# Performance work log

Hardware: AMD Instinct MI355X
Metric: run time of the kernel (lower is better)

Reference implementation:

```python
import jax, jax.numpy as jnp
import numpy as np

IN_FEATURES = 1024
OUT_FEATURES = 4096
POOL_K = 4
SCALE = 2.0
M = 32768


def setup_inputs() -> dict:
    key = jax.random.key(0)
    kx, kw, kb = jax.random.split(key, 3)
    bound = 1.0 / np.sqrt(IN_FEATURES)
    x = jax.random.normal(kx, (M, IN_FEATURES), dtype=jnp.float32)
    weight = jax.random.uniform(kw, (OUT_FEATURES, IN_FEATURES), dtype=jnp.float32, minval=-bound, maxval=bound)
    bias = jax.random.uniform(kb, (OUT_FEATURES,), dtype=jnp.float32, minval=-bound, maxval=bound)
    return {"x": x, "weight": weight, "bias": bias}


def _tanh_gelu(x):
    # tanh approximation of GELU, matching the Triton epilogue
    c = 0.7978845608028654  # sqrt(2/pi)
    return 0.5 * x * (1.0 + jnp.tanh(c * (x + 0.044715 * x * x * x)))


def reference(x, weight, bias):
    k = POOL_K
    n_pool = (OUT_FEATURES - k) // k + 1  # avgpool1d output length
    n_eff = n_pool * k
    # Fold AvgPool1d into weight/bias: avg over pooling groups
    w_pooled = weight[:n_eff].reshape(n_pool, k, IN_FEATURES).mean(axis=1)  # [N_pool, K]
    b_pooled = bias[:n_eff].reshape(n_pool, k).mean(axis=1)                  # [N_pool]
    y = jnp.einsum('mk,nk->mn', x, w_pooled) + b_pooled[None, :]             # [M, N_pool]
    y = _tanh_gelu(y) * SCALE
    return jnp.max(y, axis=1)  # [M]
```

## Files before the change

kernel.cpp:

```cpp
#include <hip/hip_runtime.h>
#include <hip/hip_bf16.h>

#define M_DIM 32768
#define K_DIM 1024
#define N_POOL 1024

#define BM 128
#define BN 128
#define BK 64

typedef __attribute__((ext_vector_type(8))) short bf16x8;
typedef __attribute__((ext_vector_type(4))) float f32x4;

typedef __attribute__((address_space(3))) unsigned int lds_uint;
typedef const __attribute__((address_space(1))) unsigned int g_uint;

__device__ __forceinline__ unsigned short f2bf(float f) {
    unsigned int u = __builtin_bit_cast(unsigned int, f);
    unsigned int lsb = (u >> 16) & 1u;
    u += 0x7fffu + lsb;
    return (unsigned short)(u >> 16);
}

__device__ __forceinline__ unsigned int f2bf2(float lo, float hi) {
    __hip_bfloat162 h2 = __float22bfloat162_rn(make_float2(lo, hi));
    union { __hip_bfloat162 h; unsigned int u; } c;
    c.h = h2;
    return c.u;
}

__global__ __launch_bounds__(256) void prep_kernel(
        const float* __restrict__ W, const float* __restrict__ b,
        unsigned short* __restrict__ wp, float* __restrict__ bp) {
    int n = blockIdx.x;
    int t = threadIdx.x;
    const float4* r0 = (const float4*)(W + (size_t)(4 * n + 0) * K_DIM);
    const float4* r1 = (const float4*)(W + (size_t)(4 * n + 1) * K_DIM);
    const float4* r2 = (const float4*)(W + (size_t)(4 * n + 2) * K_DIM);
    const float4* r3 = (const float4*)(W + (size_t)(4 * n + 3) * K_DIM);
    float4 a0 = r0[t], a1 = r1[t], a2 = r2[t], a3 = r3[t];
    float sx = (a0.x + a1.x + a2.x + a3.x) * 0.25f;
    float sy = (a0.y + a1.y + a2.y + a3.y) * 0.25f;
    float sz = (a0.z + a1.z + a2.z + a3.z) * 0.25f;
    float sw = (a0.w + a1.w + a2.w + a3.w) * 0.25f;
    ushort4 h;
    h.x = f2bf(sx); h.y = f2bf(sy); h.z = f2bf(sz); h.w = f2bf(sw);
    *(ushort4*)&wp[(size_t)n * K_DIM + t * 4] = h;
    if (t == 0)
        bp[n] = 0.25f * (b[4 * n] + b[4 * n + 1] + b[4 * n + 2] + b[4 * n + 3]);
}

__global__ __launch_bounds__(256, 2) void gemm_kernel(
        const float* __restrict__ x, const unsigned short* __restrict__ wp,
        const float* __restrict__ bp, float* __restrict__ partial) {
    __shared__ unsigned short As[BM * BK];
    __shared__ unsigned short Bs[BN * BK];

    int bid = blockIdx.x;
    int wg = (bid & 7) * 256 + (bid >> 3);
    int nblk = wg & 7;
    int mblk = wg >> 3;
    int m0 = mblk * BM;
    int n0 = nblk * BN;

    int tid = threadIdx.x;
    int lane = tid & 63;
    int wid = tid >> 6;
    int wr = wid >> 1, wc = wid & 1;

    f32x4 acc[4][4];
#pragma unroll
    for (int i = 0; i < 4; ++i)
#pragma unroll
        for (int j = 0; j < 4; ++j)
            acc[i][j] = (f32x4)(0.0f);

    const float4* xg = (const float4*)x;

    for (int kt = 0; kt < K_DIM / BK; ++kt) {
        __syncthreads();
#pragma unroll
        for (int i = 0; i < 4; ++i) {
            int ii = wid * 4 + i;
            int rsub = lane >> 3;
            int g = (lane & 7) ^ rsub;
            int n = n0 + ii * 8 + rsub;
            int kc = kt * BK + g * 8;
            __builtin_amdgcn_global_load_lds(
                (g_uint*)(wp + (size_t)n * K_DIM + kc),
                (lds_uint*)&Bs[ii * 512], 16, 0, 0);
        }
        float4 av[8];
#pragma unroll
        for (int j = 0; j < 4; ++j) {
            int f16 = j * 256 + tid;
            int r = f16 >> 3, c16 = f16 & 7;
            size_t base = (size_t)(m0 + r) * 256 + kt * 16 + c16 * 2;
            av[2 * j]     = xg[base];
            av[2 * j + 1] = xg[base + 1];
        }
#pragma unroll
        for (int j = 0; j < 4; ++j) {
            int f16 = j * 256 + tid;
            int r = f16 >> 3, c16 = f16 & 7;
            union { bf16x8 v; unsigned int u[4]; } pk;
            pk.u[0] = f2bf2(av[2 * j].x,     av[2 * j].y);
            pk.u[1] = f2bf2(av[2 * j].z,     av[2 * j].w);
            pk.u[2] = f2bf2(av[2 * j + 1].x, av[2 * j + 1].y);
            pk.u[3] = f2bf2(av[2 * j + 1].z, av[2 * j + 1].w);
            *(bf16x8*)&As[r * 64 + ((c16 ^ (r & 7)) << 3)] = pk.v;
        }
        __syncthreads();

#pragma unroll
        for (int kk = 0; kk < BK; kk += 32) {
            int c16r = (kk >> 3) + (lane >> 4);
            bf16x8 af[4], bff[4];
#pragma unroll
            for (int mi = 0; mi < 4; ++mi) {
                int r = wr * 64 + mi * 16 + (lane & 15);
                af[mi] = *(const bf16x8*)&As[r * 64 + ((c16r ^ (r & 7)) << 3)];
            }
#pragma unroll
            for (int ni = 0; ni < 4; ++ni) {
                int r = wc * 64 + ni * 16 + (lane & 15);
                bff[ni] = *(const bf16x8*)&Bs[r * 64 + ((c16r ^ (r & 7)) << 3)];
            }
#pragma unroll
            for (int mi = 0; mi < 4; ++mi)
#pragma unroll
                for (int ni = 0; ni < 4; ++ni)
                    acc[mi][ni] = __builtin_amdgcn_mfma_f32_16x16x32_bf16(
                        af[mi], bff[ni], acc[mi][ni], 0, 0, 0);
        }
    }

    float bv[4];
#pragma unroll
    for (int ni = 0; ni < 4; ++ni)
        bv[ni] = bp[n0 + wc * 64 + ni * 16 + (lane & 15)];

    const float GC = 0.7978845608028654f;
#pragma unroll
    for (int mi = 0; mi < 4; ++mi) {
#pragma unroll
        for (int j = 0; j < 4; ++j) {
            float mx = -3.4e38f;
#pragma unroll
            for (int ni = 0; ni < 4; ++ni) {
                float y = acc[mi][ni][j] + bv[ni];
                float z = GC * (y + 0.044715f * y * y * y);
                float e = __expf(2.0f * z);
                float th = 1.0f - 2.0f / (e + 1.0f);
                float g = y * (1.0f + th);
                mx = fmaxf(mx, g);
            }
#pragma unroll
            for (int s = 1; s < 16; s <<= 1)
                mx = fmaxf(mx, __shfl_xor(mx, s, 64));
            if ((lane & 15) == 0) {
                int grow = m0 + wr * 64 + mi * 16 + (lane >> 4) * 4 + j;
                partial[(size_t)(nblk * 2 + wc) * M_DIM + grow] = mx;
            }
        }
    }
}

__global__ __launch_bounds__(256) void reduce_kernel(
        const float* __restrict__ partial, float* __restrict__ out) {
    int m = blockIdx.x * 256 + threadIdx.x;
    float mx = -3.4e38f;
#pragma unroll
    for (int c = 0; c < 16; ++c)
        mx = fmaxf(mx, partial[(size_t)c * M_DIM + m]);
    out[m] = mx;
}

extern "C" void kernel_launch(void* const* d_in, const int* in_sizes, int n_in,
                              void* d_out, int out_size, void* d_ws, size_t ws_size,
                              hipStream_t stream) {
    const float* x = (const float*)d_in[0];
    const float* W = (const float*)d_in[1];
    const float* bias = (const float*)d_in[2];
    float* out = (float*)d_out;

    unsigned short* wp = (unsigned short*)d_ws;
    float* bp = (float*)((char*)d_ws + 2 * 1024 * 1024);
    float* partial = (float*)((char*)d_ws + 2 * 1024 * 1024 + 4096);

    prep_kernel<<<N_POOL, 256, 0, stream>>>(W, bias, wp, bp);
    gemm_kernel<<<(M_DIM / BM) * (N_POOL / BN), 256, 0, stream>>>(x, wp, bp, partial);
    reduce_kernel<<<M_DIM / 256, 256, 0, stream>>>(partial, out);
}
```

Baseline: 110.1 us.

## Enlarge GEMM tile to 256x256 with double-buffered LDS and interleaved MFMA phases

Doubles the tile size to 256x256 with 512 threads (8 waves, each computing 128x64). Shared memory is double-buffered so the global loads for the next k-tile (x converted to bf16, plus direct-to-LDS weight loads) are issued while MFMAs run on the current tile. The compute is split into four quadrant phases separated by barriers and setprio hints. The larger tile means the fp32 x data is read fewer times across N blocks. In exchange it uses 128KB of LDS, which may hurt occupancy since launch_bounds(512,2) likely cannot be met, and it raises register pressure from 32 accumulators per thread.

```diff
diff --git a/kernel.cpp b/kernel.cpp
--- a/kernel.cpp
+++ b/kernel.cpp
@@ -5,9 +5,10 @@
 #define K_DIM 1024
 #define N_POOL 1024
 
-#define BM 128
-#define BN 128
+#define BM 256
+#define BN 256
 #define BK 64
+#define KTILES (K_DIM / BK)
 
 typedef __attribute__((ext_vector_type(8))) short bf16x8;
 typedef __attribute__((ext_vector_type(4))) float f32x4;
@@ -50,99 +51,193 @@
         bp[n] = 0.25f * (b[4 * n] + b[4 * n + 1] + b[4 * n + 2] + b[4 * n + 3]);
 }
 
-__global__ __launch_bounds__(256, 2) void gemm_kernel(
+
+__device__ __forceinline__ bf16x8 ldfrag(const unsigned short* base, int r, int c16) {
+    return *(const bf16x8*)&base[r * 64 + (((c16) ^ (r & 7)) << 3)];
+}
+
+struct AStage { float4 av[8]; };
+
+__device__ __forceinline__ void a_issue(AStage& s, const float4* __restrict__ xg,
+                                        int m0, int kc, int tid) {
+#pragma unroll
+    for (int j = 0; j < 4; ++j) {
+        int p = j * 512 + tid;
+        int row = p >> 3, c16 = p & 7;
+        size_t base = (size_t)(m0 + row) * 256 + (kc >> 2) + c16 * 2;
+        s.av[2 * j]     = xg[base];
+        s.av[2 * j + 1] = xg[base + 1];
+    }
+}
+
+__device__ __forceinline__ void a_write(const AStage& s, unsigned short* An, int tid) {
+#pragma unroll
+    for (int j = 0; j < 4; ++j) {
+        int p = j * 512 + tid;
+        int row = p >> 3, c16 = p & 7;
+        union { bf16x8 v; unsigned int u[4]; } pk;
+        pk.u[0] = f2bf2(s.av[2 * j].x,     s.av[2 * j].y);
+        pk.u[1] = f2bf2(s.av[2 * j].z,     s.av[2 * j].w);
+        pk.u[2] = f2bf2(s.av[2 * j + 1].x, s.av[2 * j + 1].y);
+        pk.u[3] = f2bf2(s.av[2 * j + 1].z, s.av[2 * j + 1].w);
+        *(bf16x8*)&An[row * 64 + ((c16 ^ (row & 7)) << 3)] = pk.v;
+    }
+}
+
+__device__ __forceinline__ void b_issue(const unsigned short* __restrict__ wp,
+                                        unsigned short* Bn, int n0, int kc,
+                                        int wid, int lane) {
+#pragma unroll
+    for (int i = 0; i < 4; ++i) {
+        int row0 = (wid * 4 + i) * 8;
+        int n = n0 + row0 + (lane >> 3);
+        int g = (lane & 7) ^ (lane >> 3);
+        __builtin_amdgcn_global_load_lds(
+            (g_uint*)(wp + (size_t)n * K_DIM + kc + g * 8),
+            (lds_uint*)&Bn[row0 * 64], 16, 0, 0);
+    }
+}
+
+__global__ __launch_bounds__(512, 2) void gemm_kernel(
         const float* __restrict__ x, const unsigned short* __restrict__ wp,
         const float* __restrict__ bp, float* __restrict__ partial) {
-    __shared__ unsigned short As[BM * BK];
-    __shared__ unsigned short Bs[BN * BK];
+    __shared__ unsigned short As[2][BM * BK];
+    __shared__ unsigned short Bs[2][BN * BK];
 
     int bid = blockIdx.x;
-    int wg = (bid & 7) * 256 + (bid >> 3);
-    int nblk = wg & 7;
-    int mblk = wg >> 3;
+    int wg = (bid & 7) * 64 + (bid >> 3);
+    int nblk = wg & 3;
+    int mblk = wg >> 2;
     int m0 = mblk * BM;
     int n0 = nblk * BN;
 
     int tid = threadIdx.x;
     int lane = tid & 63;
     int wid = tid >> 6;
-    int wr = wid >> 1, wc = wid & 1;
-
-    f32x4 acc[4][4];
-#pragma unroll
-    for (int i = 0; i < 4; ++i)
+    int wm = wid >> 2, wn = wid & 3;
+    int rl = lane & 15;
+    int q = lane >> 4;
+
+    f32x4 acc[8][4];
+#pragma unroll
+    for (int i = 0; i < 8; ++i)
 #pragma unroll
         for (int j = 0; j < 4; ++j)
             acc[i][j] = (f32x4)(0.0f);
 
     const float4* xg = (const float4*)x;
 
-    for (int kt = 0; kt < K_DIM / BK; ++kt) {
-        __syncthreads();
-#pragma unroll
-        for (int i = 0; i < 4; ++i) {
-            int ii = wid * 4 + i;
-            int rsub = lane >> 3;
-            int g = (lane & 7) ^ rsub;
-            int n = n0 + ii * 8 + rsub;
-            int kc = kt * BK + g * 8;
-            __builtin_amdgcn_global_load_lds(
-                (g_uint*)(wp + (size_t)n * K_DIM + kc),
-                (lds_uint*)&Bs[ii * 512], 16, 0, 0);
+    {
+        AStage sa;
+        a_issue(sa, xg, m0, 0, tid);
+        b_issue(wp, Bs[0], n0, 0, wid, lane);
+        a_write(sa, As[0], tid);
+        asm volatile("s_waitcnt vmcnt(0) lgkmcnt(0)" ::: "memory");
+        __builtin_amdgcn_sched_barrier(0);
+        __builtin_amdgcn_s_barrier();
+    }
+
+#pragma unroll 1
+    for (int kt = 0; kt < KTILES; ++kt) {
+        const int cur = kt & 1;
+        const bool stage = (kt + 1) < KTILES;
+        const int kc = (kt + 1) * BK;
+        const unsigned short* Ac = As[cur];
+        const unsigned short* Bc = Bs[cur];
+        unsigned short* An = As[cur ^ 1];
+        unsigned short* Bn = Bs[cur ^ 1];
+
+        bf16x8 af0[4][2], af1[4][2], bf0[2][2], bf1[2][2];
+        AStage sa;
+
+#pragma unroll
+        for (int mi = 0; mi < 4; ++mi)
+#pragma unroll
+            for (int ks = 0; ks < 2; ++ks)
+                af0[mi][ks] = ldfrag(Ac, wm * 128 + mi * 16 + rl, ks * 4 + q);
+#pragma unroll
+        for (int ni = 0; ni < 2; ++ni)
+#pragma unroll
+            for (int ks = 0; ks < 2; ++ks)
+                bf0[ni][ks] = ldfrag(Bc, wn * 64 + ni * 16 + rl, ks * 4 + q);
+        if (stage) {
+            a_issue(sa, xg, m0, kc, tid);
+            b_issue(wp, Bn, n0, kc, wid, lane);
         }
-        float4 av[8];
-#pragma unroll
-        for (int j = 0; j < 4; ++j) {
-            int f16 = j * 256 + tid;
-            int r = f16 >> 3, c16 = f16 & 7;
-            size_t base = (size_t)(m0 + r) * 256 + kt * 16 + c16 * 2;
-            av[2 * j]     = xg[base];
-            av[2 * j + 1] = xg[base + 1];
-        }
-#pragma unroll
-        for (int j = 0; j < 4; ++j) {
-            int f16 = j * 256 + tid;
-            int r = f16 >> 3, c16 = f16 & 7;
-            union { bf16x8 v; unsigned int u[4]; } pk;
-            pk.u[0] = f2bf2(av[2 * j].x,     av[2 * j].y);
-            pk.u[1] = f2bf2(av[2 * j].z,     av[2 * j].w);
-            pk.u[2] = f2bf2(av[2 * j + 1].x, av[2 * j + 1].y);
-            pk.u[3] = f2bf2(av[2 * j + 1].z, av[2 * j + 1].w);
-            *(bf16x8*)&As[r * 64 + ((c16 ^ (r & 7)) << 3)] = pk.v;
-        }
-        __syncthreads();
-
-#pragma unroll
-        for (int kk = 0; kk < BK; kk += 32) {
-            int c16r = (kk >> 3) + (lane >> 4);
-            bf16x8 af[4], bff[4];
-#pragma unroll
-            for (int mi = 0; mi < 4; ++mi) {
-                int r = wr * 64 + mi * 16 + (lane & 15);
-                af[mi] = *(const bf16x8*)&As[r * 64 + ((c16r ^ (r & 7)) << 3)];
-            }
-#pragma unroll
-            for (int ni = 0; ni < 4; ++ni) {
-                int r = wc * 64 + ni * 16 + (lane & 15);
-                bff[ni] = *(const bf16x8*)&Bs[r * 64 + ((c16r ^ (r & 7)) << 3)];
-            }
-#pragma unroll
-            for (int mi = 0; mi < 4; ++mi)
-#pragma unroll
-                for (int ni = 0; ni < 4; ++ni)
+        __builtin_amdgcn_s_barrier();
+        __builtin_amdgcn_s_setprio(1);
+#pragma unroll
+        for (int ks = 0; ks < 2; ++ks)
+#pragma unroll
+            for (int mi = 0; mi < 4; ++mi)
+#pragma unroll
+                for (int ni = 0; ni < 2; ++ni)
                     acc[mi][ni] = __builtin_amdgcn_mfma_f32_16x16x32_bf16(
-                        af[mi], bff[ni], acc[mi][ni], 0, 0, 0);
-        }
+                        af0[mi][ks], bf0[ni][ks], acc[mi][ni], 0, 0, 0);
+        __builtin_amdgcn_s_setprio(0);
+        __builtin_amdgcn_s_barrier();
+
+#pragma unroll
+        for (int ni = 0; ni < 2; ++ni)
+#pragma unroll
+            for (int ks = 0; ks < 2; ++ks)
+                bf1[ni][ks] = ldfrag(Bc, wn * 64 + (ni + 2) * 16 + rl, ks * 4 + q);
+        __builtin_amdgcn_s_barrier();
+        __builtin_amdgcn_s_setprio(1);
+#pragma unroll
+        for (int ks = 0; ks < 2; ++ks)
+#pragma unroll
+            for (int mi = 0; mi < 4; ++mi)
+#pragma unroll
+                for (int ni = 0; ni < 2; ++ni)
+                    acc[mi][ni + 2] = __builtin_amdgcn_mfma_f32_16x16x32_bf16(
+                        af0[mi][ks], bf1[ni][ks], acc[mi][ni + 2], 0, 0, 0);
+        __builtin_amdgcn_s_setprio(0);
+        __builtin_amdgcn_s_barrier();
+
+#pragma unroll
+        for (int mi = 0; mi < 4; ++mi)
+#pragma unroll
+            for (int ks = 0; ks < 2; ++ks)
+                af1[mi][ks] = ldfrag(Ac, wm * 128 + (mi + 4) * 16 + rl, ks * 4 + q);
+        if (stage)
+            a_write(sa, An, tid);
+        __builtin_amdgcn_s_barrier();
+        __builtin_amdgcn_s_setprio(1);
+#pragma unroll
+        for (int ks = 0; ks < 2; ++ks)
+#pragma unroll
+            for (int mi = 0; mi < 4; ++mi)
+#pragma unroll
+                for (int ni = 0; ni < 2; ++ni)
+                    acc[mi + 4][ni + 2] = __builtin_amdgcn_mfma_f32_16x16x32_bf16(
+                        af1[mi][ks], bf1[ni][ks], acc[mi + 4][ni + 2], 0, 0, 0);
+        __builtin_amdgcn_s_setprio(0);
+        __builtin_amdgcn_s_barrier();
+
+        __builtin_amdgcn_s_setprio(1);
+#pragma unroll
+        for (int ks = 0; ks < 2; ++ks)
+#pragma unroll
+            for (int mi = 0; mi < 4; ++mi)
+#pragma unroll
+                for (int ni = 0; ni < 2; ++ni)
+                    acc[mi + 4][ni] = __builtin_amdgcn_mfma_f32_16x16x32_bf16(
+                        af1[mi][ks], bf0[ni][ks], acc[mi + 4][ni], 0, 0, 0);
+        __builtin_amdgcn_s_setprio(0);
+        asm volatile("s_waitcnt vmcnt(0) lgkmcnt(0)" ::: "memory");
+        __builtin_amdgcn_sched_barrier(0);
+        __builtin_amdgcn_s_barrier();
     }
 
     float bv[4];
 #pragma unroll
     for (int ni = 0; ni < 4; ++ni)
-        bv[ni] = bp[n0 + wc * 64 + ni * 16 + (lane & 15)];
+        bv[ni] = bp[n0 + wn * 64 + ni * 16 + rl];
 
     const float GC = 0.7978845608028654f;
 #pragma unroll
-    for (int mi = 0; mi < 4; ++mi) {
+    for (int mi = 0; mi < 8; ++mi) {
 #pragma unroll
         for (int j = 0; j < 4; ++j) {
             float mx = -3.4e38f;
@@ -158,9 +253,9 @@
 #pragma unroll
             for (int s = 1; s < 16; s <<= 1)
                 mx = fmaxf(mx, __shfl_xor(mx, s, 64));
-            if ((lane & 15) == 0) {
-                int grow = m0 + wr * 64 + mi * 16 + (lane >> 4) * 4 + j;
-                partial[(size_t)(nblk * 2 + wc) * M_DIM + grow] = mx;
+            if (rl == 0) {
+                int grow = m0 + wm * 128 + mi * 16 + q * 4 + j;
+                partial[(size_t)(nblk * 4 + wn) * M_DIM + grow] = mx;
             }
         }
     }
@@ -189,6 +284,6 @@
     float* partial = (float*)((char*)d_ws + 2 * 1024 * 1024 + 4096);
 
     prep_kernel<<<N_POOL, 256, 0, stream>>>(W, bias, wp, bp);
-    gemm_kernel<<<(M_DIM / BM) * (N_POOL / BN), 256, 0, stream>>>(x, wp, bp, partial);
+    gemm_kernel<<<(M_DIM / BM) * (N_POOL / BN), 512, 0, stream>>>(x, wp, bp, partial);
     reduce_kernel<<<M_DIM / 256, 256, 0, stream>>>(partial, out);
 }
```

Measured after the change: 223.9 us. 103% more time.

## Double-buffer LDS tiles to overlap next-tile global loads with MFMA compute

Applied to the files above, without the earlier changes.

Adds a second LDS buffer for the A and B tiles. Global loads for the next K-tile (fp32 x held in registers, bf16 weights sent directly to LDS) are issued before the current tile's MFMAs, and the converted A tile is written to LDS afterwards. This removes one barrier per iteration and hides global load latency behind compute. In exchange LDS use doubles to 64KB per block, which may limit occupancy to two blocks per CU. The loop also adds s_setprio around the MFMA section.

```diff
diff --git a/kernel.cpp b/kernel.cpp
--- a/kernel.cpp
+++ b/kernel.cpp
@@ -8,6 +8,7 @@
 #define BM 128
 #define BN 128
 #define BK 64
+#define KTILES (K_DIM / BK)
 
 typedef __attribute__((ext_vector_type(8))) short bf16x8;
 typedef __attribute__((ext_vector_type(4))) float f32x4;
@@ -50,11 +51,55 @@
         bp[n] = 0.25f * (b[4 * n] + b[4 * n + 1] + b[4 * n + 2] + b[4 * n + 3]);
 }
 
+
+struct AStage { float4 av[8]; };
+
+__device__ __forceinline__ void a_issue(AStage& s, const float4* __restrict__ xg,
+                                        int m0, int kt, int tid) {
+#pragma unroll
+    for (int j = 0; j < 4; ++j) {
+        int f16 = j * 256 + tid;
+        int r = f16 >> 3, c16 = f16 & 7;
+        size_t base = (size_t)(m0 + r) * 256 + kt * 16 + c16 * 2;
+        s.av[2 * j]     = xg[base];
+        s.av[2 * j + 1] = xg[base + 1];
+    }
+}
+
+__device__ __forceinline__ void a_write(const AStage& s, unsigned short* An, int tid) {
+#pragma unroll
+    for (int j = 0; j < 4; ++j) {
+        int f16 = j * 256 + tid;
+        int r = f16 >> 3, c16 = f16 & 7;
+        union { bf16x8 v; unsigned int u[4]; } pk;
+        pk.u[0] = f2bf2(s.av[2 * j].x,     s.av[2 * j].y);
+        pk.u[1] = f2bf2(s.av[2 * j].z,     s.av[2 * j].w);
+        pk.u[2] = f2bf2(s.av[2 * j + 1].x, s.av[2 * j + 1].y);
+        pk.u[3] = f2bf2(s.av[2 * j + 1].z, s.av[2 * j + 1].w);
+        *(bf16x8*)&An[r * 64 + ((c16 ^ (r & 7)) << 3)] = pk.v;
+    }
+}
+
+__device__ __forceinline__ void b_issue(const unsigned short* __restrict__ wp,
+                                        unsigned short* Bn, int n0, int kt,
+                                        int wid, int lane) {
+#pragma unroll
+    for (int i = 0; i < 4; ++i) {
+        int ii = wid * 4 + i;
+        int rsub = lane >> 3;
+        int g = (lane & 7) ^ rsub;
+        int n = n0 + ii * 8 + rsub;
+        __builtin_amdgcn_global_load_lds(
+            (g_uint*)(wp + (size_t)n * K_DIM + kt * BK + g * 8),
+            (lds_uint*)&Bn[ii * 512], 16, 0, 0);
+    }
+}
+
 __global__ __launch_bounds__(256, 2) void gemm_kernel(
         const float* __restrict__ x, const unsigned short* __restrict__ wp,
         const float* __restrict__ bp, float* __restrict__ partial) {
-    __shared__ unsigned short As[BM * BK];
-    __shared__ unsigned short Bs[BN * BK];
+    __shared__ unsigned short As[2][BM * BK];
+    __shared__ unsigned short Bs[2][BN * BK];
 
     int bid = blockIdx.x;
     int wg = (bid & 7) * 256 + (bid >> 3);
@@ -77,40 +122,30 @@
 
     const float4* xg = (const float4*)x;
 
-    for (int kt = 0; kt < K_DIM / BK; ++kt) {
-        __syncthreads();
-#pragma unroll
-        for (int i = 0; i < 4; ++i) {
-            int ii = wid * 4 + i;
-            int rsub = lane >> 3;
-            int g = (lane & 7) ^ rsub;
-            int n = n0 + ii * 8 + rsub;
-            int kc = kt * BK + g * 8;
-            __builtin_amdgcn_global_load_lds(
-                (g_uint*)(wp + (size_t)n * K_DIM + kc),
-                (lds_uint*)&Bs[ii * 512], 16, 0, 0);
+    {
+        AStage sa;
+        a_issue(sa, xg, m0, 0, tid);
+        b_issue(wp, Bs[0], n0, 0, wid, lane);
+        a_write(sa, As[0], tid);
+        asm volatile("s_waitcnt vmcnt(0) lgkmcnt(0)" ::: "memory");
+        __builtin_amdgcn_sched_barrier(0);
+        __builtin_amdgcn_s_barrier();
+    }
+
+#pragma unroll 1
+    for (int kt = 0; kt < KTILES; ++kt) {
+        const int cur = kt & 1;
+        const bool stage = (kt + 1) < KTILES;
+        const unsigned short* Ac = As[cur];
+        const unsigned short* Bc = Bs[cur];
+        unsigned short* An = As[cur ^ 1];
+        unsigned short* Bn = Bs[cur ^ 1];
+
+        AStage sa;
+        if (stage) {
+            a_issue(sa, xg, m0, kt + 1, tid);
+            b_issue(wp, Bn, n0, kt + 1, wid, lane);
         }
-        float4 av[8];
-#pragma unroll
-        for (int j = 0; j < 4; ++j) {
-            int f16 = j * 256 + tid;
-            int r = f16 >> 3, c16 = f16 & 7;
-            size_t base = (size_t)(m0 + r) * 256 + kt * 16 + c16 * 2;
-            av[2 * j]     = xg[base];
-            av[2 * j + 1] = xg[base + 1];
-        }
-#pragma unroll
-        for (int j = 0; j < 4; ++j) {
-            int f16 = j * 256 + tid;
-            int r = f16 >> 3, c16 = f16 & 7;
-            union { bf16x8 v; unsigned int u[4]; } pk;
-            pk.u[0] = f2bf2(av[2 * j].x,     av[2 * j].y);
-            pk.u[1] = f2bf2(av[2 * j].z,     av[2 * j].w);
-            pk.u[2] = f2bf2(av[2 * j + 1].x, av[2 * j + 1].y);
-            pk.u[3] = f2bf2(av[2 * j + 1].z, av[2 * j + 1].w);
-            *(bf16x8*)&As[r * 64 + ((c16 ^ (r & 7)) << 3)] = pk.v;
-        }
-        __syncthreads();
 
 #pragma unroll
         for (int kk = 0; kk < BK; kk += 32) {
@@ -119,20 +154,29 @@
 #pragma unroll
             for (int mi = 0; mi < 4; ++mi) {
                 int r = wr * 64 + mi * 16 + (lane & 15);
-                af[mi] = *(const bf16x8*)&As[r * 64 + ((c16r ^ (r & 7)) << 3)];
+                af[mi] = *(const bf16x8*)&Ac[r * 64 + ((c16r ^ (r & 7)) << 3)];
             }
 #pragma unroll
             for (int ni = 0; ni < 4; ++ni) {
                 int r = wc * 64 + ni * 16 + (lane & 15);
-                bff[ni] = *(const bf16x8*)&Bs[r * 64 + ((c16r ^ (r & 7)) << 3)];
-            }
+                bff[ni] = *(const bf16x8*)&Bc[r * 64 + ((c16r ^ (r & 7)) << 3)];
+            }
+            __builtin_amdgcn_s_setprio(1);
 #pragma unroll
             for (int mi = 0; mi < 4; ++mi)
 #pragma unroll
                 for (int ni = 0; ni < 4; ++ni)
                     acc[mi][ni] = __builtin_amdgcn_mfma_f32_16x16x32_bf16(
                         af[mi], bff[ni], acc[mi][ni], 0, 0, 0);
+            __builtin_amdgcn_s_setprio(0);
         }
+
+        if (stage)
+            a_write(sa, An, tid);
+
+        asm volatile("s_waitcnt vmcnt(0) lgkmcnt(0)" ::: "memory");
+        __builtin_amdgcn_sched_barrier(0);
+        __builtin_amdgcn_s_barrier();
     }
 
     float bv[4];
```

New measurement: 154.3 us. +40.1%, slower.

## Pre-convert x to swizzled bf16 tiles and load A via direct-to-LDS loads

Applied to the files above, without the earlier changes.

A separate kernel converts the fp32 input to bf16 once, writing it in a tile-contiguous, XOR-swizzled layout. The GEMM then fills A tiles with global_load_lds like B, removing the per-block register load, conversion and LDS store that was repeated for each of the 8 column blocks. In exchange it adds a full extra pass over x (read fp32, write bf16) and extra workspace.

```diff
diff --git a/kernel.cpp b/kernel.cpp
--- a/kernel.cpp
+++ b/kernel.cpp
@@ -8,6 +8,7 @@
 #define BM 128
 #define BN 128
 #define BK 64
+#define KTILES (K_DIM / BK)
 
 typedef __attribute__((ext_vector_type(8))) short bf16x8;
 typedef __attribute__((ext_vector_type(4))) float f32x4;
@@ -50,8 +51,66 @@
         bp[n] = 0.25f * (b[4 * n] + b[4 * n + 1] + b[4 * n + 2] + b[4 * n + 3]);
 }
 
+__global__ __launch_bounds__(256) void conv_kernel(
+        const float* __restrict__ x, unsigned short* __restrict__ xb) {
+    int bid = blockIdx.x;
+    int mblk = bid >> 3;
+    int sub = bid & 7;
+    int m0 = mblk * BM;
+    int tid = threadIdx.x;
+    size_t tb = (size_t)mblk * 16 * 8192;
+#pragma unroll
+    for (int j = 0; j < 8; ++j) {
+        int p = sub * 2048 + j * 256 + tid;
+        int kt = p >> 10;
+        int r = (p >> 3) & 127;
+        int c16 = p & 7;
+        const float4* src = (const float4*)(x + (size_t)(m0 + r) * K_DIM + kt * 64 + c16 * 8);
+        float4 a = src[0], b = src[1];
+        union { bf16x8 v; unsigned int u[4]; } pk;
+        pk.u[0] = f2bf2(a.x, a.y);
+        pk.u[1] = f2bf2(a.z, a.w);
+        pk.u[2] = f2bf2(b.x, b.y);
+        pk.u[3] = f2bf2(b.z, b.w);
+        *(bf16x8*)&xb[tb + (size_t)kt * 8192 + r * 64 + ((c16 ^ (r & 7)) << 3)] = pk.v;
+    }
+}
+
+
+__device__ __forceinline__ bf16x8 ldfrag(const unsigned short* base, int r, int c16) {
+    return *(const bf16x8*)&base[r * 64 + (((c16) ^ (r & 7)) << 3)];
+}
+
+__device__ __forceinline__ void a_issue(const unsigned short* __restrict__ xb,
+                                        unsigned short* As, int mblk, int kt,
+                                        int wid, int lane) {
+    size_t base = ((size_t)mblk * 16 + kt) * 8192;
+#pragma unroll
+    for (int i = 0; i < 4; ++i) {
+        int c = i * 256 + wid * 64 + lane;
+        __builtin_amdgcn_global_load_lds(
+            (g_uint*)(xb + base + (size_t)c * 8),
+            (lds_uint*)&As[(i * 256 + wid * 64) * 8], 16, 0, 0);
+    }
+}
+
+__device__ __forceinline__ void b_issue(const unsigned short* __restrict__ wp,
+                                        unsigned short* Bs, int n0, int kt,
+                                        int wid, int lane) {
+#pragma unroll
+    for (int i = 0; i < 4; ++i) {
+        int ii = wid * 4 + i;
+        int rsub = lane >> 3;
+        int g = (lane & 7) ^ rsub;
+        int n = n0 + ii * 8 + rsub;
+        __builtin_amdgcn_global_load_lds(
+            (g_uint*)(wp + (size_t)n * K_DIM + kt * BK + g * 8),
+            (lds_uint*)&Bs[ii * 512], 16, 0, 0);
+    }
+}
+
 __global__ __launch_bounds__(256, 2) void gemm_kernel(
-        const float* __restrict__ x, const unsigned short* __restrict__ wp,
+        const unsigned short* __restrict__ xb, const unsigned short* __restrict__ wp,
         const float* __restrict__ bp, float* __restrict__ partial) {
     __shared__ unsigned short As[BM * BK];
     __shared__ unsigned short Bs[BN * BK];
@@ -60,7 +119,6 @@
     int wg = (bid & 7) * 256 + (bid >> 3);
     int nblk = wg & 7;
     int mblk = wg >> 3;
-    int m0 = mblk * BM;
     int n0 = nblk * BN;
 
     int tid = threadIdx.x;
@@ -75,41 +133,11 @@
         for (int j = 0; j < 4; ++j)
             acc[i][j] = (f32x4)(0.0f);
 
-    const float4* xg = (const float4*)x;
-
-    for (int kt = 0; kt < K_DIM / BK; ++kt) {
+#pragma unroll 1
+    for (int kt = 0; kt < KTILES; ++kt) {
         __syncthreads();
-#pragma unroll
-        for (int i = 0; i < 4; ++i) {
-            int ii = wid * 4 + i;
-            int rsub = lane >> 3;
-            int g = (lane & 7) ^ rsub;
-            int n = n0 + ii * 8 + rsub;
-            int kc = kt * BK + g * 8;
-            __builtin_amdgcn_global_load_lds(
-                (g_uint*)(wp + (size_t)n * K_DIM + kc),
-                (lds_uint*)&Bs[ii * 512], 16, 0, 0);
-        }
-        float4 av[8];
-#pragma unroll
-        for (int j = 0; j < 4; ++j) {
-            int f16 = j * 256 + tid;
-            int r = f16 >> 3, c16 = f16 & 7;
-            size_t base = (size_t)(m0 + r) * 256 + kt * 16 + c16 * 2;
-            av[2 * j]     = xg[base];
-            av[2 * j + 1] = xg[base + 1];
-        }
-#pragma unroll
-        for (int j = 0; j < 4; ++j) {
-            int f16 = j * 256 + tid;
-            int r = f16 >> 3, c16 = f16 & 7;
-            union { bf16x8 v; unsigned int u[4]; } pk;
-            pk.u[0] = f2bf2(av[2 * j].x,     av[2 * j].y);
-            pk.u[1] = f2bf2(av[2 * j].z,     av[2 * j].w);
-            pk.u[2] = f2bf2(av[2 * j + 1].x, av[2 * j + 1].y);
-            pk.u[3] = f2bf2(av[2 * j + 1].z, av[2 * j + 1].w);
-            *(bf16x8*)&As[r * 64 + ((c16 ^ (r & 7)) << 3)] = pk.v;
-        }
+        a_issue(xb, As, mblk, kt, wid, lane);
+        b_issue(wp, Bs, n0, kt, wid, lane);
         __syncthreads();
 
 #pragma unroll
@@ -119,12 +147,12 @@
 #pragma unroll
             for (int mi = 0; mi < 4; ++mi) {
                 int r = wr * 64 + mi * 16 + (lane & 15);
-                af[mi] = *(const bf16x8*)&As[r * 64 + ((c16r ^ (r & 7)) << 3)];
+                af[mi] = ldfrag(As, r, c16r);
             }
 #pragma unroll
             for (int ni = 0; ni < 4; ++ni) {
                 int r = wc * 64 + ni * 16 + (lane & 15);
-                bff[ni] = *(const bf16x8*)&Bs[r * 64 + ((c16r ^ (r & 7)) << 3)];
+                bff[ni] = ldfrag(Bs, r, c16r);
             }
 #pragma unroll
             for (int mi = 0; mi < 4; ++mi)
@@ -135,6 +163,7 @@
         }
     }
 
+    int m0 = mblk * BM;
     float bv[4];
 #pragma unroll
     for (int ni = 0; ni < 4; ++ni)
@@ -187,8 +216,10 @@
     unsigned short* wp = (unsigned short*)d_ws;
     float* bp = (float*)((char*)d_ws + 2 * 1024 * 1024);
     float* partial = (float*)((char*)d_ws + 2 * 1024 * 1024 + 4096);
-
+    unsigned short* xb = (unsigned short*)((char*)d_ws + 8 * 1024 * 1024);
+
+    conv_kernel<<<2048, 256, 0, stream>>>(x, xb);
     prep_kernel<<<N_POOL, 256, 0, stream>>>(W, bias, wp, bp);
-    gemm_kernel<<<(M_DIM / BM) * (N_POOL / BN), 256, 0, stream>>>(x, wp, bp, partial);
+    gemm_kernel<<<(M_DIM / BM) * (N_POOL / BN), 256, 0, stream>>>(xb, wp, bp, partial);
     reduce_kernel<<<M_DIM / 256, 256, 0, stream>>>(partial, out);
 }
```

Result: slower. 124.0 us (+12.6%).
